# Kernel tuning notes

Hardware: AMD Instinct MI355X
Metric: run time of the kernel (lower is better)

## Reference

```python
import jax, jax.numpy as jnp
import numpy as np

EPS = 1e-5


def _ln(x, g, b):
    m = jnp.mean(x, axis=-1, keepdims=True)
    v = jnp.var(x, axis=-1, keepdims=True)
    return (x - m) * jax.lax.rsqrt(v + EPS) * g + b


def setup_inputs() -> dict:
    key = jax.random.key(0)
    B, N, C, H = 1, 384, 128, 128
    ks = jax.random.split(key, 8)

    def lin(k, fan_in, fan_out):
        return (jax.random.normal(k, (fan_in, fan_out), jnp.float32)
                / np.float32(np.sqrt(fan_in)))

    return {
        "pair": jax.random.normal(ks[0], (B, N, N, C), jnp.float32),
        # LayerNorm params
        "g_left": jnp.ones((C,), jnp.float32), "b_left": jnp.zeros((C,), jnp.float32),
        "g_right": jnp.ones((C,), jnp.float32), "b_right": jnp.zeros((C,), jnp.float32),
        "g_out": jnp.ones((C,), jnp.float32), "b_out": jnp.zeros((C,), jnp.float32),
        # Linear params (stored as (in, out))
        "W_l": lin(ks[1], C, H), "bias_l": jnp.zeros((H,), jnp.float32),
        "W_r": lin(ks[2], C, H), "bias_r": jnp.zeros((H,), jnp.float32),
        "W_g": lin(ks[3], C, H), "bias_g": jnp.zeros((H,), jnp.float32),
        "W_e": lin(ks[4], C, H), "bias_e": jnp.zeros((H,), jnp.float32),
        "W_o": lin(ks[5], H, C), "bias_o": jnp.zeros((C,), jnp.float32),
    }


def reference(pair, g_left, b_left, g_right, b_right, g_out, b_out,
              W_l, bias_l, W_r, bias_r, W_g, bias_g, W_e, bias_e,
              W_o, bias_o):
    # pair: (B, N, N, C)
    left = _ln(pair, g_left, b_left) @ W_l + bias_l        # (B,N,N,H)
    right = _ln(pair, g_right, b_right) @ W_r + bias_r     # (B,N,N,H)
    gate = jax.nn.sigmoid(pair @ W_g + bias_g)             # (B,N,N,H)
    left = left + pair @ W_e + bias_e                      # eq branch
    # triangular multiplication: contract over k per hidden channel
    out = jnp.einsum('bikh,bkjh->bijh', left, right)       # (B,N,N,H)
    out = out * gate
    out = out @ W_o + bias_o                               # (B,N,N,C)
    return _ln(out + pair, g_out, b_out)
```

## Files before the change

### kernel.cpp

```cpp
#include <hip/hip_runtime.h>

#define N_  384
#define C_  128
#define NN_ (N_*N_)

typedef __bf16 bf16x8 __attribute__((ext_vector_type(8)));
typedef float  floatx4 __attribute__((ext_vector_type(4)));

__device__ inline unsigned short f2bf(float f) {
    __bf16 h = (__bf16)f;
    return __builtin_bit_cast(unsigned short, h);
}

__global__ void prep(
    const float* __restrict__ Wl, const float* __restrict__ Wr,
    const float* __restrict__ Wg, const float* __restrict__ We,
    const float* __restrict__ gl, const float* __restrict__ bl,
    const float* __restrict__ gr, const float* __restrict__ br,
    const float* __restrict__ bsl, const float* __restrict__ bse,
    const float* __restrict__ bsr,
    __bf16* __restrict__ WtL, __bf16* __restrict__ WtE,
    __bf16* __restrict__ WtR, __bf16* __restrict__ WtG,
    float* __restrict__ cL, float* __restrict__ cR,
    float* __restrict__ sEw, float* __restrict__ sGw)
{
    const int b = blockIdx.x, t = threadIdx.x;
    if (b < 4) {
        const float* W  = (b==0) ? Wl  : (b==1) ? We  : (b==2) ? Wr  : Wg;
        __bf16*      Wt = (b==0) ? WtL : (b==1) ? WtE : (b==2) ? WtR : WtG;
        float scale = (b==0) ? gl[t] : (b==2) ? gr[t] : 1.f;
        for (int h = 0; h < C_; ++h)
            Wt[(size_t)h*C_ + t] = (__bf16)(W[(size_t)t*C_ + h] * scale);
    } else {
        float aL = 0.f, aR = 0.f, aE = 0.f, aG = 0.f;
        for (int c = 0; c < C_; ++c) {
            aL += bl[c] * Wl[(size_t)c*C_ + t];
            aR += br[c] * Wr[(size_t)c*C_ + t];
            aE += We[(size_t)c*C_ + t];
            aG += Wg[(size_t)c*C_ + t];
        }
        cL[t]  = aL + bsl[t] + bse[t];
        cR[t]  = aR + bsr[t];
        sEw[t] = aE;
        sGw[t] = aG;
    }
}

__global__ __launch_bounds__(256) void p_proj(
    const float* __restrict__ pair,
    const __bf16* __restrict__ WtL, const __bf16* __restrict__ WtE,
    const __bf16* __restrict__ WtR, const __bf16* __restrict__ WtG,
    const float* __restrict__ cL, const float* __restrict__ cR,
    const float* __restrict__ sEw, const float* __restrict__ sGw,
    const float* __restrict__ bsg,
    int h0,
    __bf16* __restrict__ leftC, __bf16* __restrict__ rightC,
    __bf16* __restrict__ gateC)
{
    __shared__ __align__(16) __bf16 sY[64][128];
    __shared__ __align__(16) __bf16 sW4[4][32][128];
    __shared__ __align__(16) __bf16 sT[32][72];
    __shared__ float sM[64], sIv[64];

    const int t = threadIdx.x;
    const int rid0 = blockIdx.x * 64;
    const int lane = t & 63, w = t >> 6;
    const int l15 = lane & 15, quad = lane >> 4;

    {
        const int r = t >> 2, seg = t & 3;
        const float* prow = pair + (size_t)(rid0 + r) * C_;
        float4 xv[8];
        float s = 0.f, sq = 0.f;
        #pragma unroll
        for (int u = 0; u < 8; ++u) {
            xv[u] = *(const float4*)(prow + u*16 + seg*4);
            s  += xv[u].x + xv[u].y + xv[u].z + xv[u].w;
            sq += xv[u].x*xv[u].x + xv[u].y*xv[u].y
                + xv[u].z*xv[u].z + xv[u].w*xv[u].w;
        }
        s  += __shfl_xor(s, 1);  s  += __shfl_xor(s, 2);
        sq += __shfl_xor(sq, 1); sq += __shfl_xor(sq, 2);
        float m  = s * (1.f/128.f);
        float v  = sq * (1.f/128.f) - m*m;
        float rs = rsqrtf(v + 1e-5f);
        if (seg == 0) { sM[r] = m; sIv[r] = 1.f / rs; }
        #pragma unroll
        for (int u = 0; u < 8; ++u) {
            int c0 = u*16 + seg*4;
            int dst = (((c0 >> 3) ^ (r & 7)) << 3) + (c0 & 7);
            union { unsigned short us[4]; uint2 v2; } py;
            py.us[0] = f2bf((xv[u].x - m)*rs);
            py.us[1] = f2bf((xv[u].y - m)*rs);
            py.us[2] = f2bf((xv[u].z - m)*rs);
            py.us[3] = f2bf((xv[u].w - m)*rs);
            *(uint2*)&sY[r][dst] = py.v2;
        }
    }

    for (int half = 0; half < 2; ++half) {
        const int hb = h0 + half*32;
        {
            const int hh = t >> 3, c8 = t & 7;
            const __bf16* srcs[4] = {
                WtL + (size_t)(hb + hh)*C_, WtE + (size_t)(hb + hh)*C_,
                WtR + (size_t)(hb + hh)*C_, WtG + (size_t)(hb + hh)*C_ };
            #pragma unroll
            for (int mat = 0; mat < 4; ++mat) {
                #pragma unroll
                for (int rep = 0; rep < 2; ++rep) {
                    int cc = c8 + rep*8;
                    *(uint4*)&sW4[mat][hh][((cc ^ (hh & 7)) << 3)] =
                        *(const uint4*)(srcs[mat] + cc*8);
                }
            }
        }
        __syncthreads();

        floatx4 aL[2] = {}, aE[2] = {}, aR[2] = {}, aG[2] = {};
        #pragma unroll
        for (int ks = 0; ks < 4; ++ks) {
            const int cs = ((ks*4 + quad) ^ (l15 & 7)) << 3;
            bf16x8 af = *(const bf16x8*)&sY[w*16 + l15][cs];
            #pragma unroll
            for (int nt = 0; nt < 2; ++nt) {
                const int hr = nt*16 + l15;
                aL[nt] = __builtin_amdgcn_mfma_f32_16x16x32_bf16(
                    af, *(const bf16x8*)&sW4[0][hr][cs], aL[nt], 0, 0, 0);
                aE[nt] = __builtin_amdgcn_mfma_f32_16x16x32_bf16(
                    af, *(const bf16x8*)&sW4[1][hr][cs], aE[nt], 0, 0, 0);
                aR[nt] = __builtin_amdgcn_mfma_f32_16x16x32_bf16(
                    af, *(const bf16x8*)&sW4[2][hr][cs], aR[nt], 0, 0, 0);
                aG[nt] = __builtin_amdgcn_mfma_f32_16x16x32_bf16(
                    af, *(const bf16x8*)&sW4[3][hr][cs], aG[nt], 0, 0, 0);
            }
        }

        #pragma unroll
        for (int nt = 0; nt < 2; ++nt) {
            const int hl_ = nt*16 + l15;
            const float se = sEw[hb + hl_], clv = cL[hb + hl_];
            #pragma unroll
            for (int reg = 0; reg < 4; ++reg) {
                const int rr = w*16 + quad*4 + reg;
                sT[hl_][rr] = (__bf16)(aL[nt][reg] + sIv[rr]*aE[nt][reg]
                                       + sM[rr]*se + clv);
            }
        }
        __syncthreads();
        {
            const int hh = t >> 3, sg = t & 7;
            *(uint4*)(leftC + (size_t)(half*32 + hh)*NN_ + rid0 + sg*8) =
                *(const uint4*)&sT[hh][sg*8];
        }
        __syncthreads();

        #pragma unroll
        for (int nt = 0; nt < 2; ++nt) {
            const int hl_ = nt*16 + l15;
            const float crv = cR[hb + hl_];
            #pragma unroll
            for (int reg = 0; reg < 4; ++reg) {
                const int rr = w*16 + quad*4 + reg;
                sT[hl_][rr] = (__bf16)(aR[nt][reg] + crv);
            }
        }
        __syncthreads();
        {
            const int hh = t >> 3, sg = t & 7;
            *(uint4*)(rightC + (size_t)(half*32 + hh)*NN_ + rid0 + sg*8) =
                *(const uint4*)&sT[hh][sg*8];
        }
        __syncthreads();

        #pragma unroll
        for (int nt = 0; nt < 2; ++nt) {
            const int hl_ = nt*16 + l15;
            const float sg_ = sGw[hb + hl_], bg = bsg[hb + hl_];
            #pragma unroll
            for (int reg = 0; reg < 4; ++reg) {
                const int rr = w*16 + quad*4 + reg;
                float z = sIv[rr]*aG[nt][reg] + sM[rr]*sg_ + bg;
                sT[hl_][rr] = (__bf16)(1.f / (1.f + expf(-z)));
            }
        }
        __syncthreads();
        {
            const int hh = t >> 3, sg = t & 7;
            *(uint4*)(gateC + (size_t)(half*32 + hh)*NN_ + rid0 + sg*8) =
                *(const uint4*)&sT[hh][sg*8];
        }
        __syncthreads();
    }
}

__global__ __launch_bounds__(256) void t_right(__bf16* __restrict__ p)
{
    __shared__ __align__(16) __bf16 tA[64][72];
    __shared__ __align__(16) __bf16 tB[64][72];
    const int plane = blockIdx.x / 21;
    int rem = blockIdx.x % 21, ri = 0;
    while (rem >= 6 - ri) { rem -= 6 - ri; ++ri; }
    const int ci = ri + rem;
    __bf16* base = p + (size_t)plane * NN_;
    const int t = threadIdx.x;
    const int r = t >> 2, c0 = (t & 3) * 16;

    {
        const __bf16* srcA = base + (size_t)(ri*64 + r)*N_ + ci*64 + c0;
        *(uint4*)&tA[r][c0]   = *(const uint4*)(srcA);
        *(uint4*)&tA[r][c0+8] = *(const uint4*)(srcA + 8);
        if (ri != ci) {
            const __bf16* srcB = base + (size_t)(ci*64 + r)*N_ + ri*64 + c0;
            *(uint4*)&tB[r][c0]   = *(const uint4*)(srcB);
            *(uint4*)&tB[r][c0+8] = *(const uint4*)(srcB + 8);
        }
    }
    __syncthreads();
    {
        union { unsigned short us[8]; uint4 v; } o0, o1;
        #pragma unroll
        for (int u = 0; u < 8; ++u) {
            o0.us[u] = __builtin_bit_cast(unsigned short, tA[c0+u][r]);
            o1.us[u] = __builtin_bit_cast(unsigned short, tA[c0+8+u][r]);
        }
        __bf16* dA = base + (size_t)(ci*64 + r)*N_ + ri*64 + c0;
        *(uint4*)(dA)     = o0.v;
        *(uint4*)(dA + 8) = o1.v;
        if (ri != ci) {
            union { unsigned short us[8]; uint4 v; } p0, p1;
            #pragma unroll
            for (int u = 0; u < 8; ++u) {
                p0.us[u] = __builtin_bit_cast(unsigned short, tB[c0+u][r]);
                p1.us[u] = __builtin_bit_cast(unsigned short, tB[c0+8+u][r]);
            }
            __bf16* dB = base + (size_t)(ri*64 + r)*N_ + ci*64 + c0;
            *(uint4*)(dB)     = p0.v;
            *(uint4*)(dB + 8) = p1.v;
        }
    }
}

__global__ __launch_bounds__(256) void k_einsum(
    const __bf16* __restrict__ leftC, const __bf16* __restrict__ rightC,
    const __bf16* __restrict__ gate, __bf16* __restrict__ outG)
{
    __shared__ __align__(16) __bf16 sA[128][40];
    __shared__ __align__(16) __bf16 sB[128][40];
    __shared__ __align__(16) __bf16 sGate[128][136];

    const int bid = blockIdx.x;
    const int hl = bid / 9, t9 = bid % 9;
    const int ti = (t9 / 3) * 128, tj = (t9 % 3) * 128;
    const int tid = threadIdx.x, lane = tid & 63, w = tid >> 6;
    const int l15 = lane & 15, quad = lane >> 4;
    const size_t hNN = (size_t)hl * NN_;

    const int ar = (lane >> 2);
    const int ac = (lane & 3) * 8;
    const __bf16* gA = leftC  + hNN + (size_t)ti * N_;
    const __bf16* gB = rightC + hNN + (size_t)tj * N_;

    floatx4 acc[4][4] = {};

    for (int ks = 0; ks < 12; ++ks) {
        const int kc = ks * 32;
        uint4 va[2], vb[2];
        #pragma unroll
        for (int it = 0; it < 2; ++it) {
            int row = w*32 + it*16 + ar;
            va[it] = *(const uint4*)(gA + (size_t)row*N_ + kc + ac);
            vb[it] = *(const uint4*)(gB + (size_t)row*N_ + kc + ac);
        }
        #pragma unroll
        for (int it = 0; it < 2; ++it) {
            int row = w*32 + it*16 + ar;
            *(uint4*)&sA[row][ac] = va[it];
            *(uint4*)&sB[row][ac] = vb[it];
        }
        __syncthreads();
        bf16x8 af[4], bfr[4];
        #pragma unroll
        for (int mt = 0; mt < 4; ++mt)
            af[mt] = *(const bf16x8*)&sA[(w&1)*64 + mt*16 + l15][quad*8];
        #pragma unroll
        for (int nt = 0; nt < 4; ++nt)
            bfr[nt] = *(const bf16x8*)&sB[(w>>1)*64 + nt*16 + l15][quad*8];
        #pragma unroll
        for (int mt = 0; mt < 4; ++mt)
            #pragma unroll
            for (int nt = 0; nt < 4; ++nt)
                acc[mt][nt] = __builtin_amdgcn_mfma_f32_16x16x32_bf16(
                    af[mt], bfr[nt], acc[mt][nt], 0, 0, 0);
        __syncthreads();
    }

    #pragma unroll
    for (int it = 0; it < 8; ++it) {
        int cid = it*256 + tid;
        int ri = cid >> 4, c8 = cid & 15;
        *(uint4*)&sGate[ri][c8*8] =
            *(const uint4*)(gate + hNN + (size_t)(ti + ri)*N_ + tj + c8*8);
    }
    __syncthreads();

    const int ib = (w & 1) * 64, jbw = (w >> 1) * 64;
    #pragma unroll
    for (int mt = 0; mt < 4; ++mt) {
        const int i_base = ib + mt*16 + quad*4;
        #pragma unroll
        for (int nt = 0; nt < 4; ++nt) {
            const int j_loc = jbw + nt*16 + l15;
            union { unsigned short us[4]; uint2 v; } p;
            #pragma unroll
            for (int rr = 0; rr < 4; ++rr) {
                float g = (float)sGate[i_base + rr][j_loc];
                p.us[rr] = f2bf(acc[mt][nt][rr] * g);
            }
            *(uint2*)(outG + hNN + (size_t)(tj + j_loc)*N_ + ti + i_base) = p.v;
        }
    }
}

__global__ __launch_bounds__(256) void p_out(
    const __bf16* __restrict__ outG, const float* __restrict__ Wo,
    const float* __restrict__ bso,  const float* __restrict__ pair,
    const float* __restrict__ go,   const float* __restrict__ bo,
    float* __restrict__ out)
{
    __shared__ __align__(16) __bf16 sOh[64][128];
    __shared__ __align__(16) __bf16 sWo[128][128];

    const int t = threadIdx.x;
    const int j  = blockIdx.x / 6;
    const int i0 = (blockIdx.x % 6) * 64;
    const int lane = t & 63, w = t >> 6;
    const int l15 = lane & 15, quad = lane >> 4;

    {
        const int h = t >> 1, ibase = (t & 1) * 32;
        const __bf16* src = outG + (size_t)h*NN_ + (size_t)j*N_ + i0 + ibase;
        #pragma unroll
        for (int u = 0; u < 4; ++u) {
            uint4 vv = *(const uint4*)(src + u*8);
            const unsigned short* pv = (const unsigned short*)&vv;
            #pragma unroll
            for (int k = 0; k < 8; ++k) {
                int i = ibase + u*8 + k;
                sOh[i][(((h >> 3) ^ (i & 7)) << 3) + (h & 7)] =
                    __builtin_bit_cast(__bf16, pv[k]);
            }
        }
    }
    {
        const int h = t >> 1, cbase = (t & 1) * 64;
        const float* src = Wo + (size_t)h*C_ + cbase;
        #pragma unroll
        for (int u = 0; u < 16; ++u) {
            float4 wv = *(const float4*)(src + u*4);
            const float* wf = (const float*)&wv;
            #pragma unroll
            for (int k = 0; k < 4; ++k) {
                int c = cbase + u*4 + k;
                sWo[c][(((h >> 3) ^ (c & 7)) << 3) + (h & 7)] = (__bf16)wf[k];
            }
        }
    }
    __syncthreads();

    floatx4 acc[8] = {};
    #pragma unroll
    for (int ks = 0; ks < 4; ++ks) {
        const int cs = ((ks*4 + quad) ^ (l15 & 7)) << 3;
        bf16x8 af = *(const bf16x8*)&sOh[w*16 + l15][cs];
        #pragma unroll
        for (int nt = 0; nt < 8; ++nt)
            acc[nt] = __builtin_amdgcn_mfma_f32_16x16x32_bf16(
                af, *(const bf16x8*)&sWo[nt*16 + l15][cs], acc[nt], 0, 0, 0);
    }

    float bsov[8], gov[8], bov[8];
    #pragma unroll
    for (int nt = 0; nt < 8; ++nt) {
        const int c = nt*16 + l15;
        bsov[nt] = bso[c]; gov[nt] = go[c]; bov[nt] = bo[c];
    }

    #pragma unroll
    for (int reg = 0; reg < 4; ++reg) {
        const int i = i0 + w*16 + quad*4 + reg;
        const float* prow = pair + ((size_t)i*N_ + j)*C_;
        float zz[8];
        float ssum = 0.f, ssq = 0.f;
        #pragma unroll
        for (int nt = 0; nt < 8; ++nt) {
            float zv = acc[nt][reg] + bsov[nt] + prow[nt*16 + l15];
            zz[nt] = zv; ssum += zv; ssq += zv*zv;
        }
        #pragma unroll
        for (int d = 1; d < 16; d <<= 1) {
            ssum += __shfl_xor(ssum, d);
            ssq  += __shfl_xor(ssq, d);
        }
        const float mm = ssum * (1.f/128.f);
        const float vv = ssq * (1.f/128.f) - mm*mm;
        const float rr = rsqrtf(vv + 1e-5f);
        float* orow = out + ((size_t)i*N_ + j)*C_;
        #pragma unroll
        for (int nt = 0; nt < 8; ++nt)
            orow[nt*16 + l15] = (zz[nt] - mm)*rr*gov[nt] + bov[nt];
    }
}

extern "C" void kernel_launch(void* const* d_in, const int* in_sizes, int n_in,
                              void* d_out, int out_size, void* d_ws, size_t ws_size,
                              hipStream_t stream)
{
    const float* pair    = (const float*)d_in[0];
    const float* g_left  = (const float*)d_in[1];
    const float* b_left  = (const float*)d_in[2];
    const float* g_right = (const float*)d_in[3];
    const float* b_right = (const float*)d_in[4];
    const float* g_out   = (const float*)d_in[5];
    const float* b_out   = (const float*)d_in[6];
    const float* W_l     = (const float*)d_in[7];
    const float* bias_l  = (const float*)d_in[8];
    const float* W_r     = (const float*)d_in[9];
    const float* bias_r  = (const float*)d_in[10];
    const float* W_g     = (const float*)d_in[11];
    const float* bias_g  = (const float*)d_in[12];
    const float* W_e     = (const float*)d_in[13];
    const float* bias_e  = (const float*)d_in[14];
    const float* W_o     = (const float*)d_in[15];
    const float* bias_o  = (const float*)d_in[16];

    __bf16* outG   = (__bf16*)d_ws;
    __bf16* leftC  = (__bf16*)d_out;
    __bf16* rightC = leftC + (size_t)64*NN_;
    __bf16* gateC  = leftC + (size_t)128*NN_;

    char* prepBase = (char*)d_out + ((size_t)60 << 20);
    __bf16* WtL = (__bf16*)prepBase;
    __bf16* WtE = WtL + 16384;
    __bf16* WtR = WtL + 32768;
    __bf16* WtG = WtL + 49152;
    float*  cL  = (float*)(WtL + 65536);
    float*  cR  = cL + 128;
    float*  sEw = cL + 256;
    float*  sGw = cL + 384;

    prep<<<5, 128, 0, stream>>>(W_l, W_r, W_g, W_e,
                                g_left, b_left, g_right, b_right,
                                bias_l, bias_e, bias_r,
                                WtL, WtE, WtR, WtG, cL, cR, sEw, sGw);

    for (int h0 = 0; h0 < 128; h0 += 64) {
        p_proj<<<NN_/64, 256, 0, stream>>>(pair, WtL, WtE, WtR, WtG,
                                           cL, cR, sEw, sGw, bias_g,
                                           h0, leftC, rightC, gateC);
        t_right<<<64*21, 256, 0, stream>>>(rightC);
        k_einsum<<<64*9, 256, 0, stream>>>(leftC, rightC, gateC,
                                           outG + (size_t)h0*NN_);
    }
    p_out<<<2304, 256, 0, stream>>>(outG, W_o, bias_o, pair, g_out, b_out,
                                    (float*)d_out);
}
```

Baseline: 354.2 us.

## Read projection weights from global, store outputs directly, and alias einsum LDS buffers

In the projection kernel, the shared-memory staging of the four weight matrices is removed and MFMA B operands are read directly from global memory (cached). The shared transpose buffer is also dropped: each lane writes its 4 outputs for left, right and gate as 8-byte stores, which removes most block barriers. The einsum kernel now aliases its A/B tiles with the gate tile in one shared buffer to cut LDS use and raise occupancy. The costs are uncoalesced 8-byte global stores, repeated global weight loads, and a possible hazard if the gate tile is written while A/B are still being read.

```diff
diff --git a/kernel.cpp b/kernel.cpp
--- a/kernel.cpp
+++ b/kernel.cpp
@@ -58,8 +58,6 @@
     __bf16* __restrict__ gateC)
 {
     __shared__ __align__(16) __bf16 sY[64][128];
-    __shared__ __align__(16) __bf16 sW4[4][32][128];
-    __shared__ __align__(16) __bf16 sT[32][72];
     __shared__ float sM[64], sIv[64];
 
     const int t = threadIdx.x;
@@ -97,100 +95,53 @@
             *(uint2*)&sY[r][dst] = py.v2;
         }
     }
+    __syncthreads();
 
     for (int half = 0; half < 2; ++half) {
         const int hb = h0 + half*32;
-        {
-            const int hh = t >> 3, c8 = t & 7;
-            const __bf16* srcs[4] = {
-                WtL + (size_t)(hb + hh)*C_, WtE + (size_t)(hb + hh)*C_,
-                WtR + (size_t)(hb + hh)*C_, WtG + (size_t)(hb + hh)*C_ };
-            #pragma unroll
-            for (int mat = 0; mat < 4; ++mat) {
-                #pragma unroll
-                for (int rep = 0; rep < 2; ++rep) {
-                    int cc = c8 + rep*8;
-                    *(uint4*)&sW4[mat][hh][((cc ^ (hh & 7)) << 3)] =
-                        *(const uint4*)(srcs[mat] + cc*8);
-                }
-            }
-        }
-        __syncthreads();
 
         floatx4 aL[2] = {}, aE[2] = {}, aR[2] = {}, aG[2] = {};
         #pragma unroll
         for (int ks = 0; ks < 4; ++ks) {
             const int cs = ((ks*4 + quad) ^ (l15 & 7)) << 3;
             bf16x8 af = *(const bf16x8*)&sY[w*16 + l15][cs];
+            const int ko = (ks*4 + quad) * 8;
             #pragma unroll
             for (int nt = 0; nt < 2; ++nt) {
-                const int hr = nt*16 + l15;
+                const size_t wrow = (size_t)(hb + nt*16 + l15)*C_ + ko;
                 aL[nt] = __builtin_amdgcn_mfma_f32_16x16x32_bf16(
-                    af, *(const bf16x8*)&sW4[0][hr][cs], aL[nt], 0, 0, 0);
+                    af, *(const bf16x8*)(WtL + wrow), aL[nt], 0, 0, 0);
                 aE[nt] = __builtin_amdgcn_mfma_f32_16x16x32_bf16(
-                    af, *(const bf16x8*)&sW4[1][hr][cs], aE[nt], 0, 0, 0);
+                    af, *(const bf16x8*)(WtE + wrow), aE[nt], 0, 0, 0);
                 aR[nt] = __builtin_amdgcn_mfma_f32_16x16x32_bf16(
-                    af, *(const bf16x8*)&sW4[2][hr][cs], aR[nt], 0, 0, 0);
+                    af, *(const bf16x8*)(WtR + wrow), aR[nt], 0, 0, 0);
                 aG[nt] = __builtin_amdgcn_mfma_f32_16x16x32_bf16(
-                    af, *(const bf16x8*)&sW4[3][hr][cs], aG[nt], 0, 0, 0);
+                    af, *(const bf16x8*)(WtG + wrow), aG[nt], 0, 0, 0);
             }
         }
 
         #pragma unroll
         for (int nt = 0; nt < 2; ++nt) {
-            const int hl_ = nt*16 + l15;
-            const float se = sEw[hb + hl_], clv = cL[hb + hl_];
+            const int hg = hb + nt*16 + l15;
+            const float se = sEw[hg], clv = cL[hg];
+            const float crv = cR[hg];
+            const float sg_ = sGw[hg], bg = bsg[hg];
+            const int rb = w*16 + quad*4;
+            union { unsigned short us[4]; uint2 v; } pL, pR, pG;
             #pragma unroll
             for (int reg = 0; reg < 4; ++reg) {
-                const int rr = w*16 + quad*4 + reg;
-                sT[hl_][rr] = (__bf16)(aL[nt][reg] + sIv[rr]*aE[nt][reg]
-                                       + sM[rr]*se + clv);
-            }
-        }
-        __syncthreads();
-        {
-            const int hh = t >> 3, sg = t & 7;
-            *(uint4*)(leftC + (size_t)(half*32 + hh)*NN_ + rid0 + sg*8) =
-                *(const uint4*)&sT[hh][sg*8];
-        }
-        __syncthreads();
-
-        #pragma unroll
-        for (int nt = 0; nt < 2; ++nt) {
-            const int hl_ = nt*16 + l15;
-            const float crv = cR[hb + hl_];
-            #pragma unroll
-            for (int reg = 0; reg < 4; ++reg) {
-                const int rr = w*16 + quad*4 + reg;
-                sT[hl_][rr] = (__bf16)(aR[nt][reg] + crv);
-            }
-        }
-        __syncthreads();
-        {
-            const int hh = t >> 3, sg = t & 7;
-            *(uint4*)(rightC + (size_t)(half*32 + hh)*NN_ + rid0 + sg*8) =
-                *(const uint4*)&sT[hh][sg*8];
-        }
-        __syncthreads();
-
-        #pragma unroll
-        for (int nt = 0; nt < 2; ++nt) {
-            const int hl_ = nt*16 + l15;
-            const float sg_ = sGw[hb + hl_], bg = bsg[hb + hl_];
-            #pragma unroll
-            for (int reg = 0; reg < 4; ++reg) {
-                const int rr = w*16 + quad*4 + reg;
+                const int rr = rb + reg;
+                pL.us[reg] = f2bf(aL[nt][reg] + sIv[rr]*aE[nt][reg]
+                                  + sM[rr]*se + clv);
+                pR.us[reg] = f2bf(aR[nt][reg] + crv);
                 float z = sIv[rr]*aG[nt][reg] + sM[rr]*sg_ + bg;
-                sT[hl_][rr] = (__bf16)(1.f / (1.f + expf(-z)));
-            }
-        }
-        __syncthreads();
-        {
-            const int hh = t >> 3, sg = t & 7;
-            *(uint4*)(gateC + (size_t)(half*32 + hh)*NN_ + rid0 + sg*8) =
-                *(const uint4*)&sT[hh][sg*8];
-        }
-        __syncthreads();
+                pG.us[reg] = f2bf(1.f / (1.f + expf(-z)));
+            }
+            const size_t off = (size_t)(half*32 + nt*16 + l15)*NN_ + rid0 + rb;
+            *(uint2*)(leftC  + off) = pL.v;
+            *(uint2*)(rightC + off) = pR.v;
+            *(uint2*)(gateC  + off) = pG.v;
+        }
     }
 }
 
@@ -245,9 +196,10 @@
     const __bf16* __restrict__ leftC, const __bf16* __restrict__ rightC,
     const __bf16* __restrict__ gate, __bf16* __restrict__ outG)
 {
-    __shared__ __align__(16) __bf16 sA[128][40];
-    __shared__ __align__(16) __bf16 sB[128][40];
-    __shared__ __align__(16) __bf16 sGate[128][136];
+    __shared__ __align__(16) unsigned char smem[128*136*2];
+    __bf16 (*sA)[40]    = (__bf16(*)[40])smem;
+    __bf16 (*sB)[40]    = (__bf16(*)[40])(smem + 128*40*2);
+    __bf16 (*sGate)[136] = (__bf16(*)[136])smem;
 
     const int bid = blockIdx.x;
     const int hl = bid / 9, t9 = bid % 9;
```

New measurement: 432.6 us. +22.1%, slower.
